# Performance work log

Measured on AMD Instinct MI355X. Metric: run time of the kernel, lower is better.

The kernel has to match this reference:

```python
import jax, jax.numpy as jnp
import numpy as np

D = 8192  # n_out, already a power of two so D_adjusted == D
BATCH = 4096


def fwht(x):
    """Unnormalized fast Walsh-Hadamard transform along axis 0 (H @ x).
    x: (D, M) -> (D, M). Loop is over log2(D) butterfly stages (structural)."""
    Dn = x.shape[0]
    M = x.shape[1]
    h = 1
    while h < Dn:
        x = x.reshape(Dn // (2 * h), 2, h, M)
        a, b = x[:, 0], x[:, 1]
        x = jnp.stack([a + b, a - b], axis=1).reshape(Dn, M)
        h *= 2
    return x


def setup_inputs() -> dict:
    key = jax.random.key(0)
    k_x, k_s1, k_s2, k_rho, k_eps = jax.random.split(key, 5)
    return {
        "x": jax.random.normal(k_x, (BATCH, 1), dtype=jnp.float32),
        "s1": jax.random.normal(k_s1, (D,), dtype=jnp.float32),
        "s2": jax.random.normal(k_s2, (D,), dtype=jnp.float32),
        "g_mu": jnp.zeros((D,), dtype=jnp.float32),
        "g_rho": jax.random.uniform(k_rho, (D,), dtype=jnp.float32) - 3.0,
        "epsilon": jax.random.normal(k_eps, (D,), dtype=jnp.float32),
    }


def reference(x, s1, s2, g_mu, g_rho, epsilon):
    # variational sample g_tilde ~ N(g_mu, softplus(g_rho)^2)
    g_sigma = jax.nn.softplus(g_rho)
    g_tilde = g_mu + g_sigma * epsilon                      # (D,)
    # W = diag(s1) @ H @ diag(g_tilde) @ H @ diag(s2)
    W = s1[:, None] * fwht(g_tilde[:, None] * fwht(jnp.diag(s2)))  # (D, D)
    # column matrix: first D entries of row-major flatten, shape (D, 1)
    w_col = W.reshape(-1)[:D]                               # (D,)
    # F.linear(x, w_col[:, None]) == x @ w_col[None, :]
    return x @ w_col[None, :]                               # (BATCH, D)
```

## Files before the change

kernel.cpp:

```cpp
#include <hip/hip_runtime.h>
#include <math.h>


#define WHVI_D 8192
#define WHVI_BATCH 4096
#define ROWS_PER_BLOCK 8

typedef float v4f __attribute__((ext_vector_type(4)));

__global__ __launch_bounds__(1024) void whvi_fused(
    const float* __restrict__ x, const float* __restrict__ s1,
    const float* __restrict__ s2, const float* __restrict__ g_mu,
    const float* __restrict__ g_rho, const float* __restrict__ eps,
    float* __restrict__ out) {
  __shared__ float s[WHVI_D];
  const int tid = threadIdx.x;

  {
    const float4* mu4 = (const float4*)g_mu;
    const float4* rh4 = (const float4*)g_rho;
    const float4* ep4 = (const float4*)eps;
    #pragma unroll
    for (int t = 0; t < 2; ++t) {
      int i = tid + t * 1024;
      float4 m = mu4[i], r = rh4[i], e = ep4[i];
      float4 g;
      g.x = m.x + (fmaxf(r.x, 0.0f) + log1pf(expf(-fabsf(r.x)))) * e.x;
      g.y = m.y + (fmaxf(r.y, 0.0f) + log1pf(expf(-fabsf(r.y)))) * e.y;
      g.z = m.z + (fmaxf(r.z, 0.0f) + log1pf(expf(-fabsf(r.z)))) * e.z;
      g.w = m.w + (fmaxf(r.w, 0.0f) + log1pf(expf(-fabsf(r.w)))) * e.w;
      ((float4*)s)[i] = g;
    }
  }

  for (int h = 1; h < WHVI_D; h <<= 1) {
    __syncthreads();
    #pragma unroll
    for (int t = 0; t < 4; ++t) {
      int p = tid + t * 1024;
      int k = p & (h - 1);
      int i = ((p - k) << 1) + k;
      float a = s[i];
      float b = s[i + h];
      s[i]     = a + b;
      s[i + h] = a - b;
    }
  }
  __syncthreads();

  const float s10 = s1[0];
  const v4f* s24 = (const v4f*)s2;
  const v4f* sh4 = (const v4f*)s;
  v4f w0 = (s10 * s24[tid]) * sh4[tid];
  v4f w1 = (s10 * s24[tid + 1024]) * sh4[tid + 1024];

  const int row0 = blockIdx.x * ROWS_PER_BLOCK;
  #pragma unroll
  for (int r = 0; r < ROWS_PER_BLOCK; ++r) {
    const int row = row0 + r;
    const float xb = x[row];
    v4f* o4 = (v4f*)(out + (size_t)row * WHVI_D);
    __builtin_nontemporal_store(xb * w0, &o4[tid]);
    __builtin_nontemporal_store(xb * w1, &o4[tid + 1024]);
  }
}

extern "C" void kernel_launch(void* const* d_in, const int* in_sizes, int n_in,
                              void* d_out, int out_size, void* d_ws, size_t ws_size,
                              hipStream_t stream) {
  const float* x     = (const float*)d_in[0];
  const float* s1    = (const float*)d_in[1];
  const float* s2    = (const float*)d_in[2];
  const float* g_mu  = (const float*)d_in[3];
  const float* g_rho = (const float*)d_in[4];
  const float* eps   = (const float*)d_in[5];
  float* out = (float*)d_out;

  whvi_fused<<<WHVI_BATCH / ROWS_PER_BLOCK, 1024, 0, stream>>>(
      x, s1, s2, g_mu, g_rho, eps, out);
}
```

Before: 162.5 us.

## Compute weight vector once in a separate kernel, then stream outer product

The fused kernel is split in two. A single-block kernel computes the Hadamard-transformed weight vector once into workspace, and a second kernel reads it and writes the batch-by-D output. Before, each of the 512 blocks redid the full 8192-point transform. The first two butterfly stages are now done in registers, which removes two shared-memory passes and their barriers. The cost is an extra kernel launch and a serial single-block phase before the bandwidth-bound streaming kernel.

Result: no change. 160.8 us (-1.0%).

```diff
diff --git a/kernel.cpp b/kernel.cpp
--- a/kernel.cpp
+++ b/kernel.cpp
@@ -8,32 +8,31 @@
 
 typedef float v4f __attribute__((ext_vector_type(4)));
 
-__global__ __launch_bounds__(1024) void whvi_fused(
-    const float* __restrict__ x, const float* __restrict__ s1,
-    const float* __restrict__ s2, const float* __restrict__ g_mu,
-    const float* __restrict__ g_rho, const float* __restrict__ eps,
-    float* __restrict__ out) {
+__global__ __launch_bounds__(1024) void whvi_make_w(
+    const float* __restrict__ s1, const float* __restrict__ s2,
+    const float* __restrict__ g_mu, const float* __restrict__ g_rho,
+    const float* __restrict__ eps, float* __restrict__ w) {
   __shared__ float s[WHVI_D];
   const int tid = threadIdx.x;
 
-  {
-    const float4* mu4 = (const float4*)g_mu;
-    const float4* rh4 = (const float4*)g_rho;
-    const float4* ep4 = (const float4*)eps;
-    #pragma unroll
-    for (int t = 0; t < 2; ++t) {
-      int i = tid + t * 1024;
-      float4 m = mu4[i], r = rh4[i], e = ep4[i];
-      float4 g;
-      g.x = m.x + (fmaxf(r.x, 0.0f) + log1pf(expf(-fabsf(r.x)))) * e.x;
-      g.y = m.y + (fmaxf(r.y, 0.0f) + log1pf(expf(-fabsf(r.y)))) * e.y;
-      g.z = m.z + (fmaxf(r.z, 0.0f) + log1pf(expf(-fabsf(r.z)))) * e.z;
-      g.w = m.w + (fmaxf(r.w, 0.0f) + log1pf(expf(-fabsf(r.w)))) * e.w;
-      ((float4*)s)[i] = g;
-    }
+  const float4* mu4 = (const float4*)g_mu;
+  const float4* rh4 = (const float4*)g_rho;
+  const float4* ep4 = (const float4*)eps;
+  #pragma unroll
+  for (int t = 0; t < 2; ++t) {
+    int i = tid + t * 1024;
+    float4 m = mu4[i], r = rh4[i], e = ep4[i];
+    float g0 = m.x + (fmaxf(r.x, 0.0f) + log1pf(expf(-fabsf(r.x)))) * e.x;
+    float g1 = m.y + (fmaxf(r.y, 0.0f) + log1pf(expf(-fabsf(r.y)))) * e.y;
+    float g2 = m.z + (fmaxf(r.z, 0.0f) + log1pf(expf(-fabsf(r.z)))) * e.z;
+    float g3 = m.w + (fmaxf(r.w, 0.0f) + log1pf(expf(-fabsf(r.w)))) * e.w;
+    float b0 = g0 + g1, b1 = g0 - g1, b2 = g2 + g3, b3 = g2 - g3;
+    float4 o;
+    o.x = b0 + b2; o.y = b1 + b3; o.z = b0 - b2; o.w = b1 - b3;
+    ((float4*)s)[i] = o;
   }
 
-  for (int h = 1; h < WHVI_D; h <<= 1) {
+  for (int h = 4; h < WHVI_D; h <<= 1) {
     __syncthreads();
     #pragma unroll
     for (int t = 0; t < 4; ++t) {
@@ -51,8 +50,17 @@
   const float s10 = s1[0];
   const v4f* s24 = (const v4f*)s2;
   const v4f* sh4 = (const v4f*)s;
-  v4f w0 = (s10 * s24[tid]) * sh4[tid];
-  v4f w1 = (s10 * s24[tid + 1024]) * sh4[tid + 1024];
+  ((v4f*)w)[tid]        = (s10 * s24[tid])        * sh4[tid];
+  ((v4f*)w)[tid + 1024] = (s10 * s24[tid + 1024]) * sh4[tid + 1024];
+}
+
+__global__ __launch_bounds__(1024) void whvi_stream(
+    const float* __restrict__ x, const float* __restrict__ w,
+    float* __restrict__ out) {
+  const int tid = threadIdx.x;
+  const v4f* w4 = (const v4f*)w;
+  const v4f w0 = w4[tid];
+  const v4f w1 = w4[tid + 1024];
 
   const int row0 = blockIdx.x * ROWS_PER_BLOCK;
   #pragma unroll
@@ -75,7 +83,8 @@
   const float* g_rho = (const float*)d_in[4];
   const float* eps   = (const float*)d_in[5];
   float* out = (float*)d_out;
+  float* w   = (float*)d_ws;
 
-  whvi_fused<<<WHVI_BATCH / ROWS_PER_BLOCK, 1024, 0, stream>>>(
-      x, s1, s2, g_mu, g_rho, eps, out);
+  whvi_make_w<<<1, 1024, 0, stream>>>(s1, s2, g_mu, g_rho, eps, w);
+  whvi_stream<<<WHVI_BATCH / ROWS_PER_BLOCK, 1024, 0, stream>>>(x, w, out);
 }
```
